# Optimization experiments

Measured on AMD Instinct MI355X. Metric: run time of the kernel, lower is better.

The kernel has to match this reference:

```python
import jax, jax.numpy as jnp
import numpy as np

N, E = 20000, 100000
D_IN, H1, C1 = 512, 8, 64   # conv1: 512 -> 8 heads x 64, concat -> 512
H2, C2 = 4, 128             # conv2: 512 -> 4 heads x 128, mean -> 128


def setup_inputs() -> dict:
    key = jax.random.key(0)
    k = jax.random.split(key, 12)
    s_in = 1.0 / np.sqrt(D_IN).astype(np.float32)
    return {
        "street_embedding": jax.random.normal(k[0], (N, D_IN), jnp.float32),
        "edge_index": jax.random.randint(k[1], (2, E), 0, N),
        "y": jax.random.randint(k[2], (N,), 0, C2),
        "train_mask": jax.random.bernoulli(k[3], 0.5, (N,)),
        "W1": jax.random.normal(k[4], (D_IN, H1 * C1), jnp.float32) * s_in,
        "att_src1": jax.random.normal(k[5], (H1, C1), jnp.float32) * 0.1,
        "att_dst1": jax.random.normal(k[6], (H1, C1), jnp.float32) * 0.1,
        "b1": jnp.zeros((H1 * C1,), jnp.float32),
        "W2": jax.random.normal(k[7], (H1 * C1, H2 * C2), jnp.float32) * s_in,
        "att_src2": jax.random.normal(k[8], (H2, C2), jnp.float32) * 0.1,
        "att_dst2": jax.random.normal(k[9], (H2, C2), jnp.float32) * 0.1,
        "b2": jnp.zeros((C2,), jnp.float32),
    }


def _gat_conv(x, W, a_src, a_dst, b, src, dst, n, H, C, concat):
    # linear transform (no bias, as in PyG GATConv's internal lin)
    xp = (x @ W).reshape(n, H, C)                      # [N,H,C]
    asrc = jnp.einsum('nhc,hc->nh', xp, a_src)         # [N,H]
    adst = jnp.einsum('nhc,hc->nh', xp, a_dst)
    e = jax.nn.leaky_relu(asrc[src] + adst[dst], 0.2)  # [E',H] edge scores
    # softmax over incoming edges per destination node
    m = jax.lax.stop_gradient(jax.ops.segment_max(e, dst, num_segments=n))
    ex = jnp.exp(e - m[dst])
    denom = jax.ops.segment_sum(ex, dst, num_segments=n)
    alpha = ex / (denom[dst] + 1e-16)                  # [E',H]
    out = jax.ops.segment_sum(alpha[:, :, None] * xp[src], dst, num_segments=n)  # [N,H,C]
    if concat:
        return out.reshape(n, H * C) + b
    return out.mean(axis=1) + b


def reference(street_embedding, edge_index, y, train_mask,
              W1, att_src1, att_dst1, b1, W2, att_src2, att_dst2, b2):
    n = street_embedding.shape[0]
    loop = jnp.arange(n)
    # PyG GATConv adds self-loops by default
    src = jnp.concatenate([edge_index[0], loop])
    dst = jnp.concatenate([edge_index[1], loop])
    # dropout layers are identity in eval mode
    h = _gat_conv(street_embedding, W1, att_src1, att_dst1, b1, src, dst, n, H1, C1, True)
    h = jax.nn.elu(h)
    out = _gat_conv(h, W2, att_src2, att_dst2, b2, src, dst, n, H2, C2, False)  # [N,C2]
    # CrossEntropyLoss, mean over train_mask nodes (weighted mean, jit-safe)
    logp = jax.nn.log_softmax(out, axis=-1)
    ce = -jnp.take_along_axis(logp, y[:, None], axis=-1)[:, 0]
    w = train_mask.astype(out.dtype)
    loss_su = jnp.sum(w * ce) / jnp.sum(w)
    return (loss_su, out)
```

## Files before the change

### kernel.cpp

```cpp
#include <hip/hip_runtime.h>
#include <cmath>

#define D_IN 512
#define HC   512
#define NH1  8
#define NC1  64
#define NH2  4
#define NC2  128
#define BM 128
#define BN 128

typedef __attribute__((ext_vector_type(8))) short short8;
typedef __attribute__((ext_vector_type(8))) unsigned short u16x8;
typedef __attribute__((ext_vector_type(4))) float f32x4;

__device__ inline ushort f2bf(float f) {
  unsigned u = __float_as_uint(f);
  return (ushort)((u + 0x7FFFu + ((u >> 16) & 1u)) >> 16);
}
__device__ inline float bf2f(ushort b) { return __uint_as_float(((unsigned)b) << 16); }

__global__ void k_cast_all(const float* __restrict__ x, ushort* __restrict__ Abf,
                           const float* __restrict__ W1, const float* __restrict__ W2,
                           ushort* __restrict__ Wt1, ushort* __restrict__ Wt2, int n4x) {
  const int KN = D_IN * HC;
  int i = blockIdx.x * blockDim.x + threadIdx.x;
  if (i < n4x) {
    float4 v = ((const float4*)x)[i];
    ushort4 r = { f2bf(v.x), f2bf(v.y), f2bf(v.z), f2bf(v.w) };
    ((ushort4*)Abf)[i] = r;
  } else {
    int idx = i - n4x;
    if (idx >= 2 * KN) return;
    const float* W = (idx < KN) ? W1 : W2;
    ushort* Wt = (idx < KN) ? Wt1 : Wt2;
    int j = (idx < KN) ? idx : idx - KN;
    int n = j / D_IN, k = j - n * D_IN;
    Wt[j] = f2bf(W[(size_t)k * HC + n]);
  }
}

template<int H>
__global__ void k_gemm_bf16(const ushort* __restrict__ A, const ushort* __restrict__ Bt,
                            ushort* __restrict__ Cbf,
                            const float* __restrict__ att_s, const float* __restrict__ att_d,
                            float* __restrict__ asrc, float* __restrict__ adst, int M) {
  constexpr int C = HC / H;
  __shared__ __align__(16) ushort As[2 * 4096];
  __shared__ __align__(16) ushort Bs[2 * 4096];
  int t = threadIdx.x;

  int nwg = gridDim.x * gridDim.y;
  int lin = blockIdx.y * gridDim.x + blockIdx.x;
  int q = nwg >> 3, r = nwg & 7;
  int xcd = lin & 7, pos = lin >> 3;
  int wg = (xcd < r ? xcd * (q + 1) : r * (q + 1) + (xcd - r) * q) + pos;
  int m0 = (wg >> 2) * BM;
  int n0 = (wg & 3) * BN;

  int wave = t >> 6, lane = t & 63;
  int ln = lane & 15, qd = lane >> 4;
  int wm = (wave >> 1) * 64, wn = (wave & 1) * 64;

  f32x4 acc[4][4] = {};

  int g = t >> 6, ct = (t >> 4) & 3, lt = t & 15;
  int rA0 = m0 + g * 16 + lt;      if (rA0 > M - 1) rA0 = M - 1;
  int rA1 = m0 + 64 + g * 16 + lt; if (rA1 > M - 1) rA1 = M - 1;
  const ushort* gA0 = A + (size_t)rA0 * D_IN + ct * 8;
  const ushort* gA1 = A + (size_t)rA1 * D_IN + ct * 8;
  const ushort* gB0 = Bt + (size_t)(n0 + g * 16 + lt) * D_IN + ct * 8;
  const ushort* gB1 = Bt + (size_t)(n0 + 64 + g * 16 + lt) * D_IN + ct * 8;

#define STAGE(buf, ko)                                                          \
  do {                                                                          \
    int lo_ = (buf) * 4096;                                                     \
    __builtin_amdgcn_global_load_lds(                                           \
        (const __attribute__((address_space(1))) void*)(gA0 + (ko)),            \
        (__attribute__((address_space(3))) void*)(As + lo_ + t * 8), 16, 0, 0); \
    __builtin_amdgcn_global_load_lds(                                           \
        (const __attribute__((address_space(1))) void*)(gA1 + (ko)),            \
        (__attribute__((address_space(3))) void*)(As + lo_ + 2048 + t * 8), 16, 0, 0); \
    __builtin_amdgcn_global_load_lds(                                           \
        (const __attribute__((address_space(1))) void*)(gB0 + (ko)),            \
        (__attribute__((address_space(3))) void*)(Bs + lo_ + t * 8), 16, 0, 0); \
    __builtin_amdgcn_global_load_lds(                                           \
        (const __attribute__((address_space(1))) void*)(gB1 + (ko)),            \
        (__attribute__((address_space(3))) void*)(Bs + lo_ + 2048 + t * 8), 16, 0, 0); \
  } while (0)

  STAGE(0, 0);
  int cur = 0;
  for (int it = 0; it < 16; ++it) {
    if (it < 15) {
      STAGE(cur ^ 1, (it + 1) * 32);
      asm volatile("s_waitcnt vmcnt(4)" ::: "memory");
    } else {
      asm volatile("s_waitcnt vmcnt(0)" ::: "memory");
    }
    __builtin_amdgcn_s_barrier();
    int lo = cur * 4096;
    short8 a[4], bb[4];
#pragma unroll
    for (int i = 0; i < 4; ++i)
      a[i] = *(const short8*)&As[lo + (((wave >> 1) * 4 + i) * 4 + qd) * 128 + ln * 8];
#pragma unroll
    for (int j = 0; j < 4; ++j)
      bb[j] = *(const short8*)&Bs[lo + (((wave & 1) * 4 + j) * 4 + qd) * 128 + ln * 8];
#pragma unroll
    for (int i = 0; i < 4; ++i)
#pragma unroll
      for (int j = 0; j < 4; ++j)
        acc[i][j] = __builtin_amdgcn_mfma_f32_16x16x32_bf16(a[i], bb[j], acc[i][j], 0, 0, 0);
    __builtin_amdgcn_s_barrier();
    cur ^= 1;
  }
#undef STAGE

#pragma unroll
  for (int i = 0; i < 4; ++i) {
#pragma unroll
    for (int reg = 0; reg < 4; ++reg) {
      int row = m0 + wm + i * 16 + qd * 4 + reg;
      if (row >= M) continue;
#pragma unroll
      for (int j = 0; j < 4; ++j)
        Cbf[(size_t)row * HC + n0 + wn + j * 16 + ln] = f2bf(acc[i][j][reg]);
    }
  }

  int colbase = n0 + wn;
  int h = colbase / C;
  float sa[4], da[4];
#pragma unroll
  for (int j = 0; j < 4; ++j) {
    int c = (colbase % C) + j * 16 + ln;
    sa[j] = att_s[h * C + c];
    da[j] = att_d[h * C + c];
  }
#pragma unroll
  for (int i = 0; i < 4; ++i) {
#pragma unroll
    for (int reg = 0; reg < 4; ++reg) {
      float ps = acc[i][0][reg] * sa[0] + acc[i][1][reg] * sa[1]
               + acc[i][2][reg] * sa[2] + acc[i][3][reg] * sa[3];
      float pd = acc[i][0][reg] * da[0] + acc[i][1][reg] * da[1]
               + acc[i][2][reg] * da[2] + acc[i][3][reg] * da[3];
#pragma unroll
      for (int o = 1; o < 16; o <<= 1) { ps += __shfl_xor(ps, o); pd += __shfl_xor(pd, o); }
      int row = m0 + wm + i * 16 + qd * 4 + reg;
      if (ln == 0 && row < M) {
        if (C == 64) {
          asrc[row * H + h] = ps; adst[row * H + h] = pd;
        } else {
          int sub = (colbase >> 6) & 1;
          asrc[(row * H + h) * 2 + sub] = ps;
          adst[(row * H + h) * 2 + sub] = pd;
        }
      }
    }
  }
}

__global__ void k_hist(const int* __restrict__ ei, int E, int Etot, int* __restrict__ cnt) {
  int e = blockIdx.x * blockDim.x + threadIdx.x;
  if (e >= Etot) return;
  int d = (e < E) ? ei[E + e] : e - E;
  atomicAdd(&cnt[d], 1);
}

__global__ void k_scan(const int* __restrict__ cnt, int* __restrict__ rowstart, int N) {
  int tid = threadIdx.x;
  int T = (N + 1023) / 1024;
  int base = tid * T;
  int sum = 0;
  for (int i = 0; i < T; ++i) { int j = base + i; if (j < N) sum += cnt[j]; }
  int lane = tid & 63, w = tid >> 6;
  int v = sum;
#pragma unroll
  for (int off = 1; off < 64; off <<= 1) {
    int u = __shfl_up(v, off);
    if (lane >= off) v += u;
  }
  __shared__ int wsum[16];
  if (lane == 63) wsum[w] = v;
  __syncthreads();
  if (tid < 16) {
    int tv = wsum[tid];
#pragma unroll
    for (int off = 1; off < 16; off <<= 1) {
      int u = __shfl_up(tv, off);
      if (tid >= off) tv += u;
    }
    wsum[tid] = tv;
  }
  __syncthreads();
  int wave_prefix = (w == 0) ? 0 : wsum[w - 1];
  int run = wave_prefix + v - sum;
  for (int i = 0; i < T; ++i) {
    int j = base + i;
    if (j < N) { rowstart[j] = run; run += cnt[j]; }
  }
  if (tid == 1023) rowstart[N] = run;
}

__global__ void k_scatter(const int* __restrict__ ei, int E, int Etot,
                          const int* __restrict__ rowstart, int* __restrict__ cursor,
                          int* __restrict__ csr_src) {
  int e = blockIdx.x * blockDim.x + threadIdx.x;
  if (e >= Etot) return;
  int s = (e < E) ? ei[e] : e - E;
  int d = (e < E) ? ei[E + e] : e - E;
  int pos = atomicAdd(&cursor[d], 1);
  csr_src[rowstart[d] + pos] = s;
}

template<int H, int MODE>
__global__ void k_agg(const int* __restrict__ rowstart, const int* __restrict__ csr_src,
                      const float* __restrict__ asrc, const float* __restrict__ adst,
                      const ushort* __restrict__ xp, ushort* __restrict__ hout,
                      float* __restrict__ out2, const float* __restrict__ bias,
                      const int* __restrict__ y, const int* __restrict__ msk,
                      float* __restrict__ acc2, int N) {
  constexpr int C = HC / H;
  int wv = threadIdx.x >> 6, lane = threadIdx.x & 63;
  int n = blockIdx.x * 4 + wv;
  if (n >= N) return;
  int h = (MODE == 1) ? (lane >> 3) : (lane >> 4);
  int beg = rowstart[n], end = rowstart[n + 1];

  float adn;
  if (MODE == 1) adn = adst[n * H + h];
  else { float2 t2 = ((const float2*)adst)[n * H + h]; adn = t2.x + t2.y; }

  float acc[8] = {};
  float wsum = 0.f;

  for (int c0 = beg; c0 < end; c0 += 64) {
    int len = end - c0; if (len > 64) len = 64;
    int ev = (lane < len) ? csr_src[c0 + lane] : 0;
    int j = 0;
    for (; j + 1 < len; j += 2) {
      int s0 = __shfl(ev, j), s1 = __shfl(ev, j + 1);
      float v0, v1;
      if (MODE == 1) { v0 = asrc[s0 * H + h]; v1 = asrc[s1 * H + h]; }
      else {
        float2 p0 = ((const float2*)asrc)[s0 * H + h];
        float2 p1 = ((const float2*)asrc)[s1 * H + h];
        v0 = p0.x + p0.y; v1 = p1.x + p1.y;
      }
      u16x8 a0 = ((const u16x8*)xp)[(size_t)s0 * 64 + lane];
      u16x8 a1 = ((const u16x8*)xp)[(size_t)s1 * 64 + lane];
      v0 += adn; v1 += adn;
      v0 = (v0 > 0.f) ? v0 : 0.2f * v0;
      v1 = (v1 > 0.f) ? v1 : 0.2f * v1;
      float w0 = __expf(v0), w1 = __expf(v1);
#pragma unroll
      for (int k = 0; k < 8; ++k)
        acc[k] += w0 * bf2f(a0[k]) + w1 * bf2f(a1[k]);
      wsum += w0 + w1;
    }
    if (j < len) {
      int s0 = __shfl(ev, j);
      float v0;
      if (MODE == 1) v0 = asrc[s0 * H + h];
      else { float2 p0 = ((const float2*)asrc)[s0 * H + h]; v0 = p0.x + p0.y; }
      u16x8 a0 = ((const u16x8*)xp)[(size_t)s0 * 64 + lane];
      v0 += adn;
      v0 = (v0 > 0.f) ? v0 : 0.2f * v0;
      float w0 = __expf(v0);
#pragma unroll
      for (int k = 0; k < 8; ++k) acc[k] += w0 * bf2f(a0[k]);
      wsum += w0;
    }
  }
  float rdn = 1.0f / (wsum + 1e-16f);
#pragma unroll
  for (int k = 0; k < 8; ++k) acc[k] *= rdn;

  if (MODE == 1) {
    int c = lane * 8;
    u16x8 rr;
#pragma unroll
    for (int k = 0; k < 8; ++k) {
      float v = acc[k] + bias[c + k];
      v = (v > 0.f) ? v : expm1f(v);
      rr[k] = f2bf(v);
    }
    ((u16x8*)hout)[(size_t)n * 64 + lane] = rr;
  } else {
#pragma unroll
    for (int k = 0; k < 8; ++k) {
      float v = acc[k];
      v += __shfl_xor(v, 16);
      v += __shfl_xor(v, 32);
      acc[k] = v * 0.25f + bias[(lane & 15) * 8 + k];
    }
    if (lane < 16) {
      int cb = lane * 8;
#pragma unroll
      for (int k = 0; k < 8; ++k) out2[(size_t)n * NC2 + cb + k] = acc[k];
    }
    float mx = acc[0];
#pragma unroll
    for (int k = 1; k < 8; ++k) mx = fmaxf(mx, acc[k]);
#pragma unroll
    for (int o = 1; o < 16; o <<= 1) mx = fmaxf(mx, __shfl_xor(mx, o));
    float e = 0.f;
#pragma unroll
    for (int k = 0; k < 8; ++k) e += __expf(acc[k] - mx);
#pragma unroll
    for (int o = 1; o < 16; o <<= 1) e += __shfl_xor(e, o);
    int yv = y[n];
    float sel = acc[0];
#pragma unroll
    for (int k = 1; k < 8; ++k) sel = ((yv & 7) == k) ? acc[k] : sel;
    float vy = __shfl(sel, yv >> 3);
    if (lane == 0 && msk[n] != 0) {
      float ce = mx + logf(e) - vy;
      int slot = n & 127;
      atomicAdd(&acc2[slot], ce);
      atomicAdd(&acc2[128 + slot], 1.0f);
    }
  }
}

__global__ void k_final(const float* __restrict__ acc2, float* __restrict__ out0) {
  int tid = threadIdx.x;
  float ce = acc2[tid], ct = acc2[128 + tid];
#pragma unroll
  for (int o = 32; o > 0; o >>= 1) { ce += __shfl_xor(ce, o); ct += __shfl_xor(ct, o); }
  __shared__ float s[4];
  if ((tid & 63) == 0) { s[(tid >> 6) * 2] = ce; s[(tid >> 6) * 2 + 1] = ct; }
  __syncthreads();
  if (tid == 0) out0[0] = (s[0] + s[2]) / (s[1] + s[3]);
}

extern "C" void kernel_launch(void* const* d_in, const int* in_sizes, int n_in,
                              void* d_out, int out_size, void* d_ws, size_t ws_size,
                              hipStream_t stream) {
  const float* x   = (const float*)d_in[0];
  const int*   ei  = (const int*)d_in[1];
  const int*   y   = (const int*)d_in[2];
  const int*   msk = (const int*)d_in[3];
  const float* W1  = (const float*)d_in[4];
  const float* as1 = (const float*)d_in[5];
  const float* ad1 = (const float*)d_in[6];
  const float* b1  = (const float*)d_in[7];
  const float* W2  = (const float*)d_in[8];
  const float* as2 = (const float*)d_in[9];
  const float* ad2 = (const float*)d_in[10];
  const float* b2  = (const float*)d_in[11];
  float* out = (float*)d_out;

  int N = in_sizes[0] / D_IN;
  int E = in_sizes[1] / 2;
  int Etot = E + N;

  float* ws = (float*)d_ws;
  size_t NF = (size_t)N * HC;
  float* asr1 = ws;
  float* adt1 = asr1 + (size_t)N * NH1;
  float* asr2 = adt1 + (size_t)N * NH1;
  float* adt2 = asr2 + (size_t)N * 2 * NH2;
  float* acc2 = adt2 + (size_t)N * 2 * NH2;
  int*   cnt    = (int*)(acc2 + 256);
  int*   cursor = cnt + N;
  size_t zero_bytes = (256 + 2 * (size_t)N) * sizeof(float);
  int*   rowstart = cursor + N;
  int*   csr_src  = rowstart + N + 1;
  ushort* xpbf = (ushort*)((((uintptr_t)(csr_src + Etot)) + 15) & ~(uintptr_t)15);
  ushort* Abf = xpbf + NF;
  ushort* Wt1 = Abf + NF;
  ushort* Wt2 = Wt1 + (size_t)D_IN * HC;

  hipMemsetAsync(acc2, 0, zero_bytes, stream);

  int n4x = (int)(NF / 4);
  int cast_total = n4x + 2 * D_IN * HC;
  k_cast_all<<<(cast_total + 255) / 256, 256, 0, stream>>>(x, Abf, W1, W2, Wt1, Wt2, n4x);

  k_hist<<<(Etot + 255) / 256, 256, 0, stream>>>(ei, E, Etot, cnt);
  k_scan<<<1, 1024, 0, stream>>>(cnt, rowstart, N);
  k_scatter<<<(Etot + 255) / 256, 256, 0, stream>>>(ei, E, Etot, rowstart, cursor, csr_src);

  dim3 ggrid(HC / BN, (N + BM - 1) / BM);
  int aggblocks = (N + 3) / 4;

  k_gemm_bf16<NH1><<<ggrid, 256, 0, stream>>>(Abf, Wt1, xpbf, as1, ad1, asr1, adt1, N);
  k_agg<NH1, 1><<<aggblocks, 256, 0, stream>>>(rowstart, csr_src, asr1, adt1, xpbf, Abf,
                                               nullptr, b1, nullptr, nullptr, nullptr, N);

  k_gemm_bf16<NH2><<<ggrid, 256, 0, stream>>>(Abf, Wt2, xpbf, as2, ad2, asr2, adt2, N);
  k_agg<NH2, 2><<<aggblocks, 256, 0, stream>>>(rowstart, csr_src, asr2, adt2, xpbf, nullptr,
                                               out + 1, b2, y, msk, acc2, N);

  k_final<<<1, 128, 0, stream>>>(acc2, out);
}
```

Baseline: 296.0 us.

## Fuse histogram into cast, simplify GEMM pipeline, split layer-1 aggregation per head

Merges the degree histogram into the cast/transposition kernel, which removes one launch. The GEMM drops its double-buffered global_load_lds pipeline and XCD-aware tile remapping in favour of a single-buffered BK=64 loop with plain __syncthreads. Layer-1 aggregation is split across 8 blocks per node group, one per head, with each lane handling one channel via scalar bf16 loads instead of 8-wide vector loads. These changes trade fewer launches and more parallelism against lost load/compute overlap in the GEMM and narrower, less coalesced gathers.

```diff
diff --git a/kernel.cpp b/kernel.cpp
--- a/kernel.cpp
+++ b/kernel.cpp
@@ -9,6 +9,7 @@
 #define NC2  128
 #define BM 128
 #define BN 128
+#define BK 64
 
 typedef __attribute__((ext_vector_type(8))) short short8;
 typedef __attribute__((ext_vector_type(8))) unsigned short u16x8;
@@ -20,23 +21,29 @@
 }
 __device__ inline float bf2f(ushort b) { return __uint_as_float(((unsigned)b) << 16); }
 
-__global__ void k_cast_all(const float* __restrict__ x, ushort* __restrict__ Abf,
-                           const float* __restrict__ W1, const float* __restrict__ W2,
-                           ushort* __restrict__ Wt1, ushort* __restrict__ Wt2, int n4x) {
+__global__ void k_pre(const float* __restrict__ x, ushort* __restrict__ Abf,
+                      const float* __restrict__ W1, const float* __restrict__ W2,
+                      ushort* __restrict__ Wt1, ushort* __restrict__ Wt2, int n4x,
+                      const int* __restrict__ ei, int E, int Etot,
+                      int* __restrict__ cnt) {
   const int KN = D_IN * HC;
   int i = blockIdx.x * blockDim.x + threadIdx.x;
   if (i < n4x) {
     float4 v = ((const float4*)x)[i];
     ushort4 r = { f2bf(v.x), f2bf(v.y), f2bf(v.z), f2bf(v.w) };
     ((ushort4*)Abf)[i] = r;
-  } else {
+  } else if (i < n4x + 2 * KN) {
     int idx = i - n4x;
-    if (idx >= 2 * KN) return;
     const float* W = (idx < KN) ? W1 : W2;
     ushort* Wt = (idx < KN) ? Wt1 : Wt2;
     int j = (idx < KN) ? idx : idx - KN;
     int n = j / D_IN, k = j - n * D_IN;
     Wt[j] = f2bf(W[(size_t)k * HC + n]);
+  } else {
+    int e = i - n4x - 2 * KN;
+    if (e >= Etot) return;
+    int d = (e < E) ? ei[E + e] : e - E;
+    atomicAdd(&cnt[d], 1);
   }
 }
 
@@ -46,18 +53,11 @@
                             const float* __restrict__ att_s, const float* __restrict__ att_d,
                             float* __restrict__ asrc, float* __restrict__ adst, int M) {
   constexpr int C = HC / H;
-  __shared__ __align__(16) ushort As[2 * 4096];
-  __shared__ __align__(16) ushort Bs[2 * 4096];
+  __shared__ __align__(16) ushort As[BM * BK];
+  __shared__ __align__(16) ushort Bs[BN * BK];
   int t = threadIdx.x;
-
-  int nwg = gridDim.x * gridDim.y;
-  int lin = blockIdx.y * gridDim.x + blockIdx.x;
-  int q = nwg >> 3, r = nwg & 7;
-  int xcd = lin & 7, pos = lin >> 3;
-  int wg = (xcd < r ? xcd * (q + 1) : r * (q + 1) + (xcd - r) * q) + pos;
-  int m0 = (wg >> 2) * BM;
-  int n0 = (wg & 3) * BN;
-
+  int m0 = blockIdx.y * BM;
+  int n0 = blockIdx.x * BN;
   int wave = t >> 6, lane = t & 63;
   int ln = lane & 15, qd = lane >> 4;
   int wm = (wave >> 1) * 64, wn = (wave & 1) * 64;
@@ -72,50 +72,43 @@
   const ushort* gB0 = Bt + (size_t)(n0 + g * 16 + lt) * D_IN + ct * 8;
   const ushort* gB1 = Bt + (size_t)(n0 + 64 + g * 16 + lt) * D_IN + ct * 8;
 
-#define STAGE(buf, ko)                                                          \
-  do {                                                                          \
-    int lo_ = (buf) * 4096;                                                     \
-    __builtin_amdgcn_global_load_lds(                                           \
-        (const __attribute__((address_space(1))) void*)(gA0 + (ko)),            \
-        (__attribute__((address_space(3))) void*)(As + lo_ + t * 8), 16, 0, 0); \
-    __builtin_amdgcn_global_load_lds(                                           \
-        (const __attribute__((address_space(1))) void*)(gA1 + (ko)),            \
-        (__attribute__((address_space(3))) void*)(As + lo_ + 2048 + t * 8), 16, 0, 0); \
-    __builtin_amdgcn_global_load_lds(                                           \
-        (const __attribute__((address_space(1))) void*)(gB0 + (ko)),            \
-        (__attribute__((address_space(3))) void*)(Bs + lo_ + t * 8), 16, 0, 0); \
-    __builtin_amdgcn_global_load_lds(                                           \
-        (const __attribute__((address_space(1))) void*)(gB1 + (ko)),            \
-        (__attribute__((address_space(3))) void*)(Bs + lo_ + 2048 + t * 8), 16, 0, 0); \
-  } while (0)
-
-  STAGE(0, 0);
-  int cur = 0;
-  for (int it = 0; it < 16; ++it) {
-    if (it < 15) {
-      STAGE(cur ^ 1, (it + 1) * 32);
-      asm volatile("s_waitcnt vmcnt(4)" ::: "memory");
-    } else {
-      asm volatile("s_waitcnt vmcnt(0)" ::: "memory");
-    }
-    __builtin_amdgcn_s_barrier();
-    int lo = cur * 4096;
-    short8 a[4], bb[4];
-#pragma unroll
-    for (int i = 0; i < 4; ++i)
-      a[i] = *(const short8*)&As[lo + (((wave >> 1) * 4 + i) * 4 + qd) * 128 + ln * 8];
-#pragma unroll
-    for (int j = 0; j < 4; ++j)
-      bb[j] = *(const short8*)&Bs[lo + (((wave & 1) * 4 + j) * 4 + qd) * 128 + ln * 8];
-#pragma unroll
-    for (int i = 0; i < 4; ++i)
+  for (int k0 = 0; k0 < D_IN; k0 += BK) {
+    __syncthreads();
+#pragma unroll
+    for (int h = 0; h < 2; ++h) {
+      int ko = k0 + h * 32;
+      int lo = h * 4096;
+      __builtin_amdgcn_global_load_lds(
+          (const __attribute__((address_space(1))) void*)(gA0 + ko),
+          (__attribute__((address_space(3))) void*)(As + lo + t * 8), 16, 0, 0);
+      __builtin_amdgcn_global_load_lds(
+          (const __attribute__((address_space(1))) void*)(gA1 + ko),
+          (__attribute__((address_space(3))) void*)(As + lo + 2048 + t * 8), 16, 0, 0);
+      __builtin_amdgcn_global_load_lds(
+          (const __attribute__((address_space(1))) void*)(gB0 + ko),
+          (__attribute__((address_space(3))) void*)(Bs + lo + t * 8), 16, 0, 0);
+      __builtin_amdgcn_global_load_lds(
+          (const __attribute__((address_space(1))) void*)(gB1 + ko),
+          (__attribute__((address_space(3))) void*)(Bs + lo + 2048 + t * 8), 16, 0, 0);
+    }
+    __syncthreads();
+#pragma unroll
+    for (int h = 0; h < 2; ++h) {
+      int lo = h * 4096;
+      short8 a[4], bb[4];
+#pragma unroll
+      for (int i = 0; i < 4; ++i)
+        a[i] = *(const short8*)&As[lo + (((wave >> 1) * 4 + i) * 4 + qd) * 128 + ln * 8];
 #pragma unroll
       for (int j = 0; j < 4; ++j)
-        acc[i][j] = __builtin_amdgcn_mfma_f32_16x16x32_bf16(a[i], bb[j], acc[i][j], 0, 0, 0);
-    __builtin_amdgcn_s_barrier();
-    cur ^= 1;
-  }
-#undef STAGE
+        bb[j] = *(const short8*)&Bs[lo + (((wave & 1) * 4 + j) * 4 + qd) * 128 + ln * 8];
+#pragma unroll
+      for (int i = 0; i < 4; ++i)
+#pragma unroll
+        for (int j = 0; j < 4; ++j)
+          acc[i][j] = __builtin_amdgcn_mfma_f32_16x16x32_bf16(a[i], bb[j], acc[i][j], 0, 0, 0);
+    }
+  }
 
 #pragma unroll
   for (int i = 0; i < 4; ++i) {
@@ -162,13 +155,6 @@
   }
 }
 
-__global__ void k_hist(const int* __restrict__ ei, int E, int Etot, int* __restrict__ cnt) {
-  int e = blockIdx.x * blockDim.x + threadIdx.x;
-  if (e >= Etot) return;
-  int d = (e < E) ? ei[E + e] : e - E;
-  atomicAdd(&cnt[d], 1);
-}
-
 __global__ void k_scan(const int* __restrict__ cnt, int* __restrict__ rowstart, int N) {
   int tid = threadIdx.x;
   int T = (N + 1023) / 1024;
@@ -215,46 +201,84 @@
   csr_src[rowstart[d] + pos] = s;
 }
 
-template<int H, int MODE>
-__global__ void k_agg(const int* __restrict__ rowstart, const int* __restrict__ csr_src,
-                      const float* __restrict__ asrc, const float* __restrict__ adst,
-                      const ushort* __restrict__ xp, ushort* __restrict__ hout,
-                      float* __restrict__ out2, const float* __restrict__ bias,
-                      const int* __restrict__ y, const int* __restrict__ msk,
-                      float* __restrict__ acc2, int N) {
-  constexpr int C = HC / H;
+__global__ void k_agg1(const int* __restrict__ rowstart, const int* __restrict__ csr_src,
+                       const float* __restrict__ asrc, const float* __restrict__ adst,
+                       const ushort* __restrict__ xp, ushort* __restrict__ hout,
+                       const float* __restrict__ bias, int N) {
   int wv = threadIdx.x >> 6, lane = threadIdx.x & 63;
-  int n = blockIdx.x * 4 + wv;
+  int s = blockIdx.x & 7;
+  int n = (blockIdx.x >> 3) * 4 + wv;
   if (n >= N) return;
-  int h = (MODE == 1) ? (lane >> 3) : (lane >> 4);
   int beg = rowstart[n], end = rowstart[n + 1];
-
-  float adn;
-  if (MODE == 1) adn = adst[n * H + h];
-  else { float2 t2 = ((const float2*)adst)[n * H + h]; adn = t2.x + t2.y; }
-
-  float acc[8] = {};
-  float wsum = 0.f;
-
+  float adn = adst[n * NH1 + s];
+  const ushort* xs = xp + (size_t)s * NC1 + lane;
+
+  float accv = 0.f, wsum = 0.f;
   for (int c0 = beg; c0 < end; c0 += 64) {
     int len = end - c0; if (len > 64) len = 64;
     int ev = (lane < len) ? csr_src[c0 + lane] : 0;
     int j = 0;
     for (; j + 1 < len; j += 2) {
       int s0 = __shfl(ev, j), s1 = __shfl(ev, j + 1);
-      float v0, v1;
-      if (MODE == 1) { v0 = asrc[s0 * H + h]; v1 = asrc[s1 * H + h]; }
-      else {
-        float2 p0 = ((const float2*)asrc)[s0 * H + h];
-        float2 p1 = ((const float2*)asrc)[s1 * H + h];
-        v0 = p0.x + p0.y; v1 = p1.x + p1.y;
-      }
-      u16x8 a0 = ((const u16x8*)xp)[(size_t)s0 * 64 + lane];
-      u16x8 a1 = ((const u16x8*)xp)[(size_t)s1 * 64 + lane];
-      v0 += adn; v1 += adn;
+      float v0 = asrc[s0 * NH1 + s] + adn;
+      float v1 = asrc[s1 * NH1 + s] + adn;
+      ushort x0 = xs[(size_t)s0 * HC];
+      ushort x1 = xs[(size_t)s1 * HC];
       v0 = (v0 > 0.f) ? v0 : 0.2f * v0;
       v1 = (v1 > 0.f) ? v1 : 0.2f * v1;
       float w0 = __expf(v0), w1 = __expf(v1);
+      accv += w0 * bf2f(x0) + w1 * bf2f(x1);
+      wsum += w0 + w1;
+    }
+    if (j < len) {
+      int s0 = __shfl(ev, j);
+      float v0 = asrc[s0 * NH1 + s] + adn;
+      ushort x0 = xs[(size_t)s0 * HC];
+      v0 = (v0 > 0.f) ? v0 : 0.2f * v0;
+      float w0 = __expf(v0);
+      accv += w0 * bf2f(x0);
+      wsum += w0;
+    }
+  }
+  float v = accv / (wsum + 1e-16f) + bias[s * NC1 + lane];
+  v = (v > 0.f) ? v : expm1f(v);
+  hout[(size_t)n * HC + s * NC1 + lane] = f2bf(v);
+}
+
+__global__ void k_agg2(const int* __restrict__ rowstart, const int* __restrict__ csr_src,
+                       const float* __restrict__ asrc, const float* __restrict__ adst,
+                       const ushort* __restrict__ xp,
+                       float* __restrict__ out2, const float* __restrict__ bias,
+                       const int* __restrict__ y, const int* __restrict__ msk,
+                       float* __restrict__ acc2, int N) {
+  constexpr int H = NH2;
+  int wv = threadIdx.x >> 6, lane = threadIdx.x & 63;
+  int n = blockIdx.x * 4 + wv;
+  if (n >= N) return;
+  int h = lane >> 4;
+  int beg = rowstart[n], end = rowstart[n + 1];
+
+  float2 t2 = ((const float2*)adst)[n * H + h];
+  float adn = t2.x + t2.y;
+
+  float acc[8] = {};
+  float wsum = 0.f;
+
+  for (int c0 = beg; c0 < end; c0 += 64) {
+    int len = end - c0; if (len > 64) len = 64;
+    int ev = (lane < len) ? csr_src[c0 + lane] : 0;
+    int j = 0;
+    for (; j + 1 < len; j += 2) {
+      int s0 = __shfl(ev, j), s1 = __shfl(ev, j + 1);
+      float2 p0 = ((const float2*)asrc)[s0 * H + h];
+      float2 p1 = ((const float2*)asrc)[s1 * H + h];
+      float v0 = p0.x + p0.y + adn;
+      float v1 = p1.x + p1.y + adn;
+      u16x8 a0 = ((const u16x8*)xp)[(size_t)s0 * 64 + lane];
+      u16x8 a1 = ((const u16x8*)xp)[(size_t)s1 * 64 + lane];
+      v0 = (v0 > 0.f) ? v0 : 0.2f * v0;
+      v1 = (v1 > 0.f) ? v1 : 0.2f * v1;
+      float w0 = __expf(v0), w1 = __expf(v1);
 #pragma unroll
       for (int k = 0; k < 8; ++k)
         acc[k] += w0 * bf2f(a0[k]) + w1 * bf2f(a1[k]);
@@ -262,11 +286,9 @@
     }
     if (j < len) {
       int s0 = __shfl(ev, j);
-      float v0;
-      if (MODE == 1) v0 = asrc[s0 * H + h];
-      else { float2 p0 = ((const float2*)asrc)[s0 * H + h]; v0 = p0.x + p0.y; }
+      float2 p0 = ((const float2*)asrc)[s0 * H + h];
+      float v0 = p0.x + p0.y + adn;
       u16x8 a0 = ((const u16x8*)xp)[(size_t)s0 * 64 + lane];
-      v0 += adn;
       v0 = (v0 > 0.f) ? v0 : 0.2f * v0;
       float w0 = __expf(v0);
 #pragma unroll
@@ -278,50 +300,38 @@
 #pragma unroll
   for (int k = 0; k < 8; ++k) acc[k] *= rdn;
 
-  if (MODE == 1) {
-    int c = lane * 8;
-    u16x8 rr;
-#pragma unroll
-    for (int k = 0; k < 8; ++k) {
-      float v = acc[k] + bias[c + k];
-      v = (v > 0.f) ? v : expm1f(v);
-      rr[k] = f2bf(v);
-    }
-    ((u16x8*)hout)[(size_t)n * 64 + lane] = rr;
-  } else {
-#pragma unroll
-    for (int k = 0; k < 8; ++k) {
-      float v = acc[k];
-      v += __shfl_xor(v, 16);
-      v += __shfl_xor(v, 32);
-      acc[k] = v * 0.25f + bias[(lane & 15) * 8 + k];
-    }
-    if (lane < 16) {
-      int cb = lane * 8;
-#pragma unroll
-      for (int k = 0; k < 8; ++k) out2[(size_t)n * NC2 + cb + k] = acc[k];
-    }
-    float mx = acc[0];
-#pragma unroll
-    for (int k = 1; k < 8; ++k) mx = fmaxf(mx, acc[k]);
-#pragma unroll
-    for (int o = 1; o < 16; o <<= 1) mx = fmaxf(mx, __shfl_xor(mx, o));
-    float e = 0.f;
-#pragma unroll
-    for (int k = 0; k < 8; ++k) e += __expf(acc[k] - mx);
-#pragma unroll
-    for (int o = 1; o < 16; o <<= 1) e += __shfl_xor(e, o);
-    int yv = y[n];
-    float sel = acc[0];
-#pragma unroll
-    for (int k = 1; k < 8; ++k) sel = ((yv & 7) == k) ? acc[k] : sel;
-    float vy = __shfl(sel, yv >> 3);
-    if (lane == 0 && msk[n] != 0) {
-      float ce = mx + logf(e) - vy;
-      int slot = n & 127;
-      atomicAdd(&acc2[slot], ce);
-      atomicAdd(&acc2[128 + slot], 1.0f);
-    }
+#pragma unroll
+  for (int k = 0; k < 8; ++k) {
+    float v = acc[k];
+    v += __shfl_xor(v, 16);
+    v += __shfl_xor(v, 32);
+    acc[k] = v * 0.25f + bias[(lane & 15) * 8 + k];
+  }
+  if (lane < 16) {
+    int cb = lane * 8;
+#pragma unroll
+    for (int k = 0; k < 8; ++k) out2[(size_t)n * NC2 + cb + k] = acc[k];
+  }
+  float mx = acc[0];
+#pragma unroll
+  for (int k = 1; k < 8; ++k) mx = fmaxf(mx, acc[k]);
+#pragma unroll
+  for (int o = 1; o < 16; o <<= 1) mx = fmaxf(mx, __shfl_xor(mx, o));
+  float e = 0.f;
+#pragma unroll
+  for (int k = 0; k < 8; ++k) e += __expf(acc[k] - mx);
+#pragma unroll
+  for (int o = 1; o < 16; o <<= 1) e += __shfl_xor(e, o);
+  int yv = y[n];
+  float sel = acc[0];
+#pragma unroll
+  for (int k = 1; k < 8; ++k) sel = ((yv & 7) == k) ? acc[k] : sel;
+  float vy = __shfl(sel, yv >> 3);
+  if (lane == 0 && msk[n] != 0) {
+    float ce = mx + logf(e) - vy;
+    int slot = n & 127;
+    atomicAdd(&acc2[slot], ce);
+    atomicAdd(&acc2[128 + slot], 1.0f);
   }
 }
 
@@ -377,23 +387,23 @@
   hipMemsetAsync(acc2, 0, zero_bytes, stream);
 
   int n4x = (int)(NF / 4);
-  int cast_total = n4x + 2 * D_IN * HC;
-  k_cast_all<<<(cast_total + 255) / 256, 256, 0, stream>>>(x, Abf, W1, W2, Wt1, Wt2, n4x);
-
-  k_hist<<<(Etot + 255) / 256, 256, 0, stream>>>(ei, E, Etot, cnt);
+  int pre_total = n4x + 2 * D_IN * HC + Etot;
+  k_pre<<<(pre_total + 255) / 256, 256, 0, stream>>>(x, Abf, W1, W2, Wt1, Wt2, n4x,
+                                                     ei, E, Etot, cnt);
+
   k_scan<<<1, 1024, 0, stream>>>(cnt, rowstart, N);
   k_scatter<<<(Etot + 255) / 256, 256, 0, stream>>>(ei, E, Etot, rowstart, cursor, csr_src);
 
   dim3 ggrid(HC / BN, (N + BM - 1) / BM);
-  int aggblocks = (N + 3) / 4;
+  int agg1blocks = 8 * ((N + 3) / 4);
+  int agg2blocks = (N + 3) / 4;
 
   k_gemm_bf16<NH1><<<ggrid, 256, 0, stream>>>(Abf, Wt1, xpbf, as1, ad1, asr1, adt1, N);
-  k_agg<NH1, 1><<<aggblocks, 256, 0, stream>>>(rowstart, csr_src, asr1, adt1, xpbf, Abf,
-                                               nullptr, b1, nullptr, nullptr, nullptr, N);
+  k_agg1<<<agg1blocks, 256, 0, stream>>>(rowstart, csr_src, asr1, adt1, xpbf, Abf, b1, N);
 
   k_gemm_bf16<NH2><<<ggrid, 256, 0, stream>>>(Abf, Wt2, xpbf, as2, ad2, asr2, adt2, N);
-  k_agg<NH2, 2><<<aggblocks, 256, 0, stream>>>(rowstart, csr_src, asr2, adt2, xpbf, nullptr,
-                                               out + 1, b2, y, msk, acc2, N);
+  k_agg2<<<agg2blocks, 256, 0, stream>>>(rowstart, csr_src, asr2, adt2, xpbf,
+                                         out + 1, b2, y, msk, acc2, N);
 
   k_final<<<1, 128, 0, stream>>>(acc2, out);
 }
```

Result: slower. 330.3 us (+11.6%).
